# Optimization experiments

Measured on AMD Instinct MI355X. Metric: run time of the kernel, lower is better.

The kernel has to match this reference:

```python
import jax, jax.numpy as jnp
import numpy as np

D_MODEL = 1024
NUM_HEADS = 16
HEAD_DIM = D_MODEL // NUM_HEADS  # 64
ROPE_BASE = 10000.0


def setup_inputs() -> dict:
    key = jax.random.key(0)
    ks = jax.random.split(key, 12)
    B, S, D = 4, 2048, D_MODEL
    scale = 1.0 / np.sqrt(D)
    inp = {
        'query': jax.random.normal(ks[0], (B, S, D), jnp.float32),
        'key': jax.random.normal(ks[1], (B, S, D), jnp.float32),
        'value': jax.random.normal(ks[2], (B, S, D), jnp.float32),
        'Wq': jax.random.normal(ks[3], (D, D), jnp.float32) * scale,
        'bq': jnp.zeros((D,), jnp.float32),
        'Wk': jax.random.normal(ks[4], (D, D), jnp.float32) * scale,
        'bk': jnp.zeros((D,), jnp.float32),
        'Wv': jax.random.normal(ks[5], (D, D), jnp.float32) * scale,
        'bv': jnp.zeros((D,), jnp.float32),
        'Wo': jax.random.normal(ks[6], (D, D), jnp.float32) * scale,
        'bo': jnp.zeros((D,), jnp.float32),
    }
    return inp


def _rope_cos_sin(seq_len, head_dim, dtype):
    inv_freq = 1.0 / (ROPE_BASE ** (jnp.arange(0, head_dim, 2, dtype=jnp.float32) / head_dim))
    t = jnp.arange(seq_len, dtype=jnp.float32)
    freqs = jnp.einsum('i,j->ij', t, inv_freq)          # [S, hd/2]
    emb = jnp.concatenate([freqs, freqs], axis=-1)      # [S, hd]
    return jnp.cos(emb).astype(dtype), jnp.sin(emb).astype(dtype)


def _rotate_half(x):
    x1, x2 = jnp.split(x, 2, axis=-1)
    return jnp.concatenate([-x2, x1], axis=-1)


def reference(query, key, value, Wq, bq, Wk, bk, Wv, bv, Wo, bo):
    B, T, D = query.shape
    H, hd = NUM_HEADS, HEAD_DIM
    # projections -> [B, H, S, hd]
    Q = (query @ Wq + bq).reshape(B, T, H, hd).transpose(0, 2, 1, 3)
    K = (key @ Wk + bk).reshape(B, -1, H, hd).transpose(0, 2, 1, 3)
    V = (value @ Wv + bv).reshape(B, -1, H, hd).transpose(0, 2, 1, 3)
    # RoPE
    cos, sin = _rope_cos_sin(T, hd, Q.dtype)            # [S, hd]
    Q = Q * cos + _rotate_half(Q) * sin
    K = K * cos + _rotate_half(K) * sin
    # attention
    scores = jnp.einsum('bhtd,bhsd->bhts', Q, K) / jnp.sqrt(jnp.asarray(hd, Q.dtype))
    attn = jax.nn.softmax(scores, axis=-1)
    context = jnp.einsum('bhts,bhsd->bhtd', attn, V)
    context = context.transpose(0, 2, 1, 3).reshape(B, T, D)
    return context @ Wo + bo
```

## Files before the change

kernel.cpp:

```cpp
#include <hip/hip_runtime.h>
#include <hip/hip_bf16.h>
#include <cstdint>
#include <cstddef>

typedef __bf16 bf16_t;
typedef __bf16 bf16x8 __attribute__((ext_vector_type(8)));
typedef __bf16 bf16x4v __attribute__((ext_vector_type(4)));
typedef __bf16 bf16x2v __attribute__((ext_vector_type(2)));
typedef float f32x4 __attribute__((ext_vector_type(4)));
typedef float f32x16 __attribute__((ext_vector_type(16)));
typedef uint32_t u32x4 __attribute__((ext_vector_type(4)));
typedef uint32_t u32x2 __attribute__((ext_vector_type(2)));

#define DEVI static __device__ __forceinline__

DEVI void gl_lds16(const void* g, void* l) {
    __builtin_amdgcn_global_load_lds((const __attribute__((address_space(1))) void*)g,
                                     (__attribute__((address_space(3))) void*)l, 16, 0, 0);
}

DEVI float fexp2(float x) {
#if __has_builtin(__builtin_amdgcn_exp2f)
    return __builtin_amdgcn_exp2f(x);
#else
    return __expf(x * 0.6931471805599453f);
#endif
}

DEVI uint32_t pkbf16(float a, float b) {
    bf16x2v t;
    t[0] = (bf16_t)a;
    t[1] = (bf16_t)b;
    return __builtin_bit_cast(uint32_t, t);
}

__global__ __launch_bounds__(256) void castk(const float* __restrict__ i0, const float* __restrict__ i1,
                                             const float* __restrict__ i2, bf16_t* __restrict__ o0,
                                             bf16_t* __restrict__ o1, bf16_t* __restrict__ o2) {
    const float* in = blockIdx.y == 0 ? i0 : blockIdx.y == 1 ? i1 : i2;
    bf16_t* out = blockIdx.y == 0 ? o0 : blockIdx.y == 1 ? o1 : o2;
    size_t i = ((size_t)blockIdx.x * 256 + threadIdx.x) * 4;
    float4 v = *(const float4*)(in + i);
    bf16x4v o;
    o[0] = (bf16_t)v.x; o[1] = (bf16_t)v.y; o[2] = (bf16_t)v.z; o[3] = (bf16_t)v.w;
    *(bf16x4v*)(out + i) = o;
}

__global__ __launch_bounds__(256) void wtrans(const float* __restrict__ W0, const float* __restrict__ W1,
                                              const float* __restrict__ W2, const float* __restrict__ W3,
                                              bf16_t* __restrict__ O0, bf16_t* __restrict__ O1,
                                              bf16_t* __restrict__ O2, bf16_t* __restrict__ O3) {
    const float* W; bf16_t* O;
    switch (blockIdx.z) {
        case 0: W = W0; O = O0; break;
        case 1: W = W1; O = O1; break;
        case 2: W = W2; O = O2; break;
        default: W = W3; O = O3; break;
    }
    __shared__ float t[32][33];
    int tx = threadIdx.x & 31, ty = threadIdx.x >> 5;
    int bx = blockIdx.x * 32, by = blockIdx.y * 32;
#pragma unroll
    for (int yy = 0; yy < 4; ++yy)
        t[ty + yy * 8][tx] = W[(size_t)(by + ty + yy * 8) * 1024 + bx + tx];
    __syncthreads();
#pragma unroll
    for (int yy = 0; yy < 4; ++yy)
        O[(size_t)(bx + ty + yy * 8) * 1024 + by + tx] = (bf16_t)t[tx][ty + yy * 8];
}

__global__ __launch_bounds__(256) void rope_tab(float* __restrict__ ctab, float* __restrict__ stab) {
    int idx = blockIdx.x * 256 + threadIdx.x;
    int s = idx >> 5, i = idx & 31;
    float inv = 1.0f / powf(10000.0f, (float)i * (1.0f / 32.0f));
    float f = (float)s * inv;
    ctab[idx] = cosf(f);
    stab[idx] = sinf(f);
}

__global__ __launch_bounds__(256) void gemm_qkv(const bf16_t* __restrict__ Xq, const bf16_t* __restrict__ Xk,
                                                const bf16_t* __restrict__ Xv, const bf16_t* __restrict__ Wqt,
                                                const bf16_t* __restrict__ Wkt, const bf16_t* __restrict__ Wvt,
                                                const float* __restrict__ bqp, const float* __restrict__ bkp,
                                                const float* __restrict__ bvp, bf16_t* __restrict__ Qo,
                                                bf16_t* __restrict__ Ko, bf16_t* __restrict__ Vo,
                                                const float* __restrict__ ctab, const float* __restrict__ stab) {
    constexpr int K = 1024;
    const int z = blockIdx.z;
    const bf16_t* A  = z == 0 ? Xq : z == 1 ? Xk : Xv;
    const bf16_t* Bt = z == 0 ? Wqt : z == 1 ? Wkt : Wvt;
    const float* bias = z == 0 ? bqp : z == 1 ? bkp : bvp;
    bf16_t* O = z == 0 ? Qo : z == 1 ? Ko : Vo;
    const float scale = z == 0 ? 0.18033688011112042f : 1.0f;

    __shared__ alignas(16) bf16_t As[128 * 64];
    __shared__ alignas(16) bf16_t Bs[128 * 64];
    const int tid = threadIdx.x;
    const int w = tid >> 6, lane = tid & 63, c = lane & 15, qd = lane >> 4;
    const int wm = w >> 1, wn = w & 1;
    const int c7 = c & 7;
    const int m0 = blockIdx.x * 128, n0 = blockIdx.y * 128;
    f32x4 acc[4][4] = {};
    for (int kt = 0; kt < K / 64; ++kt) {
#pragma unroll
        for (int l = 0; l < 4; ++l) {
            int slot = l * 256 + tid;
            int row = slot >> 3, ch = slot & 7;
            int sch = ch ^ (row & 7);
            gl_lds16(A + (size_t)(m0 + row) * K + kt * 64 + sch * 8, (char*)As + (size_t)slot * 16);
            gl_lds16(Bt + (size_t)(n0 + row) * K + kt * 64 + sch * 8, (char*)Bs + (size_t)slot * 16);
        }
        __syncthreads();
#pragma unroll
        for (int kk = 0; kk < 2; ++kk) {
            const int cs8 = (kk * 4 + qd) ^ c7;
            bf16x8 af[4], bfr[4];
#pragma unroll
            for (int i = 0; i < 4; ++i)
                af[i] = *(const bf16x8*)&As[(wm * 64 + i * 16 + c) * 64 + cs8 * 8];
#pragma unroll
            for (int j = 0; j < 4; ++j)
                bfr[j] = *(const bf16x8*)&Bs[(wn * 64 + j * 16 + c) * 64 + cs8 * 8];
#pragma unroll
            for (int i = 0; i < 4; ++i)
#pragma unroll
                for (int j = 0; j < 4; ++j)
                    acc[i][j] = __builtin_amdgcn_mfma_f32_16x16x32_bf16(af[i], bfr[j], acc[i][j], 0, 0, 0);
        }
        __syncthreads();
    }
    const int mb = m0 + wm * 64;
    const int nb = n0 + wn * 64;
    const int h = nb >> 6;
    if (z == 2) {
#pragma unroll
        for (int i = 0; i < 4; ++i) {
            int m = mb + i * 16 + qd * 4;
            int b = m >> 11, s = m & 2047;
#pragma unroll
            for (int j = 0; j < 4; ++j) {
                int d = j * 16 + c;
                float bv = bias[nb + d];
                bf16x4v v4;
#pragma unroll
                for (int r = 0; r < 4; ++r) v4[r] = (bf16_t)(acc[i][j][r] + bv);
                *(bf16x4v*)(O + ((size_t)(b * 16 + h) * 64 + d) * 2048 + s) = v4;
            }
        }
    } else {
#pragma unroll
        for (int i = 0; i < 4; ++i)
#pragma unroll
            for (int jh = 0; jh < 2; ++jh) {
                int d1 = jh * 16 + c;
                float b1 = bias[nb + d1];
                float b2 = bias[nb + d1 + 32];
#pragma unroll
                for (int r = 0; r < 4; ++r) {
                    int m = mb + i * 16 + qd * 4 + r;
                    int b = m >> 11, s = m & 2047;
                    float v1 = acc[i][jh][r] + b1;
                    float v2 = acc[i][jh + 2][r] + b2;
                    float ct = ctab[s * 32 + d1];
                    float st = stab[s * 32 + d1];
                    size_t base = ((size_t)(b * 16 + h) * 2048 + s) * 64;
                    O[base + d1]      = (bf16_t)((v1 * ct - v2 * st) * scale);
                    O[base + d1 + 32] = (bf16_t)((v2 * ct + v1 * st) * scale);
                }
            }
    }
}

__global__ __launch_bounds__(256) void gemm_out(const bf16_t* __restrict__ A, const bf16_t* __restrict__ Bt,
                                                const float* __restrict__ bias, float* __restrict__ O) {
    constexpr int K = 1024, N = 1024;
    __shared__ alignas(16) bf16_t As[128 * 64];
    __shared__ alignas(16) bf16_t Bs[128 * 64];
    const int tid = threadIdx.x;
    const int w = tid >> 6, lane = tid & 63, c = lane & 15, qd = lane >> 4;
    const int wm = w >> 1, wn = w & 1;
    const int c7 = c & 7;
    const int m0 = blockIdx.x * 128, n0 = blockIdx.y * 128;
    f32x4 acc[4][4] = {};
    for (int kt = 0; kt < K / 64; ++kt) {
#pragma unroll
        for (int l = 0; l < 4; ++l) {
            int slot = l * 256 + tid;
            int row = slot >> 3, ch = slot & 7;
            int sch = ch ^ (row & 7);
            gl_lds16(A + (size_t)(m0 + row) * K + kt * 64 + sch * 8, (char*)As + (size_t)slot * 16);
            gl_lds16(Bt + (size_t)(n0 + row) * K + kt * 64 + sch * 8, (char*)Bs + (size_t)slot * 16);
        }
        __syncthreads();
#pragma unroll
        for (int kk = 0; kk < 2; ++kk) {
            const int cs8 = (kk * 4 + qd) ^ c7;
            bf16x8 af[4], bfr[4];
#pragma unroll
            for (int i = 0; i < 4; ++i)
                af[i] = *(const bf16x8*)&As[(wm * 64 + i * 16 + c) * 64 + cs8 * 8];
#pragma unroll
            for (int j = 0; j < 4; ++j)
                bfr[j] = *(const bf16x8*)&Bs[(wn * 64 + j * 16 + c) * 64 + cs8 * 8];
#pragma unroll
            for (int i = 0; i < 4; ++i)
#pragma unroll
                for (int j = 0; j < 4; ++j)
                    acc[i][j] = __builtin_amdgcn_mfma_f32_16x16x32_bf16(af[i], bfr[j], acc[i][j], 0, 0, 0);
        }
        __syncthreads();
    }
    const int mb = m0 + wm * 64, nb = n0 + wn * 64;
#pragma unroll
    for (int i = 0; i < 4; ++i)
#pragma unroll
        for (int j = 0; j < 4; ++j) {
            int n = nb + j * 16 + c;
            float bv = bias[n];
#pragma unroll
            for (int r = 0; r < 4; ++r) {
                int m = mb + i * 16 + qd * 4 + r;
                O[(size_t)m * N + n] = acc[i][j][r] + bv;
            }
        }
}

__global__ __launch_bounds__(256, 4) void attn(const bf16_t* __restrict__ Q, const bf16_t* __restrict__ K,
                                               const bf16_t* __restrict__ Vt, bf16_t* __restrict__ ctx) {
    constexpr int S = 2048, NT = S / 64;
    __shared__ alignas(16) char smem[32768];
    const int tid = threadIdx.x, w = tid >> 6, lane = tid & 63;
    const int lo5 = lane & 31, hi = lane >> 5;
    const int rm = (lo5 >> 1) & 7;
    const int bh = blockIdx.x, q0 = blockIdx.y * 128;
    const bf16_t* Qb = Q + (size_t)bh * S * 64 + (size_t)q0 * 64;
    const bf16_t* Kb = K + (size_t)bh * S * 64;
    const bf16_t* Vb = Vt + (size_t)bh * 64 * S;
#pragma unroll
    for (int l = 0; l < 4; ++l) {
        int slot = l * 256 + tid;
        int row = slot >> 3, ch = slot & 7;
        int sch = ch ^ ((row >> 1) & 7);
        gl_lds16(Qb + (size_t)row * 64 + sch * 8, smem + (size_t)slot * 16);
    }
    __syncthreads();
    bf16x8 qf[4];
    {
        const bf16_t* Qs = (const bf16_t*)smem;
#pragma unroll
        for (int kc = 0; kc < 4; ++kc)
            qf[kc] = *(const bf16x8*)&Qs[(size_t)(w * 32 + lo5) * 64 + ((kc * 2 + hi) ^ rm) * 8];
    }
    __syncthreads();
    auto stageK = [&](int kt, int buf) {
        const int s0 = kt * 64;
        char* kbase = smem + buf * 8192;
#pragma unroll
        for (int l = 0; l < 2; ++l) {
            int slot = l * 256 + tid;
            int row = slot >> 3, ch = slot & 7;
            int sch = ch ^ ((row >> 1) & 7);
            gl_lds16(Kb + (size_t)(s0 + row) * 64 + sch * 8, kbase + (size_t)slot * 16);
        }
    };
    auto stageV = [&](int kt, int buf) {
        const int s0 = kt * 64;
        char* vbase = smem + 16384 + buf * 8192;
#pragma unroll
        for (int l = 0; l < 2; ++l) {
            int slot = l * 256 + tid;
            int row = slot >> 3, ch = slot & 7;
            int sch = ch ^ ((row >> 1) & 7);
            gl_lds16(Vb + (size_t)row * S + s0 + sch * 8, vbase + (size_t)slot * 16);
        }
    };
    f32x16 acc_o[2] = {};
    f32x16 acc_l = {};
    const f32x16 Z16 = {};
    bf16x8 ones;
    {
        u32x4 ov = {0x3F803F80u, 0x3F803F80u, 0x3F803F80u, 0x3F803F80u};
        ones = __builtin_bit_cast(bf16x8, ov);
    }
    stageK(0, 0);
    __syncthreads();
    uint32_t pkuA[2][8] = {}, pkuB[2][8] = {};
    auto window = [&](int wi, uint32_t (&pkuP)[2][8], uint32_t (&pkuN)[2][8]) {
        if (wi + 1 < NT) stageK(wi + 1, (wi + 1) & 1);
        if (wi < NT) stageV(wi, wi & 1);
        f32x16 st[2];
        if (wi < NT) {
            const bf16_t* KsC = (const bf16_t*)(smem + (wi & 1) * 8192);
#pragma unroll
            for (int kc = 0; kc < 4; ++kc) {
                bf16x8 kf[2];
#pragma unroll
                for (int sb = 0; sb < 2; ++sb)
                    kf[sb] = *(const bf16x8*)&KsC[(size_t)(sb * 32 + lo5) * 64 + ((kc * 2 + hi) ^ rm) * 8];
#pragma unroll
                for (int sb = 0; sb < 2; ++sb)
                    st[sb] = __builtin_amdgcn_mfma_f32_32x32x16_bf16(kf[sb], qf[kc],
                                                                     kc == 0 ? Z16 : st[sb], 0, 0, 0);
            }
        }
        const bf16_t* VsC = (const bf16_t*)(smem + 16384 + ((wi - 1) & 1) * 8192);
#pragma unroll
        for (int skc = 0; skc < 4; ++skc) {
            const int sb = skc >> 1, b = (skc & 1) * 4;
            if (wi < NT) {
#pragma unroll
                for (int u = 0; u < 4; ++u)
                    pkuN[sb][b + u] = pkbf16(fexp2(st[sb][2 * (b + u)]), fexp2(st[sb][2 * (b + u) + 1]));
            }
            if (wi >= 1) {
                bf16x8 vf[2];
#pragma unroll
                for (int db = 0; db < 2; ++db)
                    vf[db] = *(const bf16x8*)&VsC[(size_t)(db * 32 + lo5) * 64 + ((skc * 2 + hi) ^ rm) * 8];
                uint32_t p0 = pkuP[sb][b + 0], p1 = pkuP[sb][b + 1];
                uint32_t p2 = pkuP[sb][b + 2], p3 = pkuP[sb][b + 3];
#if __has_builtin(__builtin_amdgcn_permlane32_swap)
                u32x2 r02 = __builtin_amdgcn_permlane32_swap(p0, p2, false, false);
                u32x2 r13 = __builtin_amdgcn_permlane32_swap(p1, p3, false, false);
                u32x4 av = {r02[0], r13[0], r02[1], r13[1]};
#else
                uint32_t send0 = hi ? p0 : p2;
                uint32_t send1 = hi ? p1 : p3;
                uint32_t recv0 = __shfl_xor(send0, 32);
                uint32_t recv1 = __shfl_xor(send1, 32);
                u32x4 av = {hi ? recv0 : p0, hi ? recv1 : p1,
                            hi ? p2 : recv0, hi ? p3 : recv1};
#endif
                bf16x8 af = __builtin_bit_cast(bf16x8, av);
                acc_l = __builtin_amdgcn_mfma_f32_32x32x16_bf16(af, ones, acc_l, 0, 0, 0);
#pragma unroll
                for (int db = 0; db < 2; ++db)
                    acc_o[db] = __builtin_amdgcn_mfma_f32_32x32x16_bf16(af, vf[db], acc_o[db], 0, 0, 0);
            }
        }
        __syncthreads();
    };
    for (int wi = 0; wi < NT; wi += 2) {
        window(wi, pkuB, pkuA);
        window(wi + 1, pkuA, pkuB);
    }
    window(NT, pkuB, pkuA);
    const int b = bh >> 4, h = bh & 15;
    float linv[16];
#pragma unroll
    for (int r = 0; r < 16; ++r) linv[r] = 1.0f / acc_l[r];
#pragma unroll
    for (int db = 0; db < 2; ++db)
#pragma unroll
        for (int r = 0; r < 16; ++r) {
            int qrow = q0 + w * 32 + (r & 3) + 8 * (r >> 2) + 4 * hi;
            int d = db * 32 + lo5;
            float o = acc_o[db][r] * linv[r];
            ctx[((size_t)(b * 2048 + qrow)) * 1024 + (size_t)h * 64 + d] = (bf16_t)o;
        }
}

extern "C" void kernel_launch(void* const* d_in, const int* in_sizes, int n_in,
                              void* d_out, int out_size, void* d_ws, size_t ws_size,
                              hipStream_t stream) {
    (void)in_sizes; (void)n_in; (void)out_size; (void)ws_size;
    const float* query = (const float*)d_in[0];
    const float* key   = (const float*)d_in[1];
    const float* value = (const float*)d_in[2];
    const float* Wq = (const float*)d_in[3];
    const float* bq = (const float*)d_in[4];
    const float* Wk = (const float*)d_in[5];
    const float* bk = (const float*)d_in[6];
    const float* Wv = (const float*)d_in[7];
    const float* bv = (const float*)d_in[8];
    const float* Wo = (const float*)d_in[9];
    const float* bo = (const float*)d_in[10];

    const size_t SZ = (size_t)8192 * 1024;
    bf16_t* Xq = (bf16_t*)d_ws;
    bf16_t* Xk = Xq + SZ;
    bf16_t* Xv = Xk + SZ;
    bf16_t* Qb = Xv + SZ;
    bf16_t* Kb = Qb + SZ;
    bf16_t* Vtb = Kb + SZ;
    bf16_t* Wqt = Vtb + SZ;
    bf16_t* Wkt = Wqt + 1024 * 1024;
    bf16_t* Wvt = Wkt + 1024 * 1024;
    bf16_t* Wot = Wvt + 1024 * 1024;
    float* ctab = (float*)(Wot + 1024 * 1024);
    float* stab = ctab + 2048 * 32;
    bf16_t* CT = Xq;

    castk<<<dim3(8192, 3), 256, 0, stream>>>(query, key, value, Xq, Xk, Xv);
    wtrans<<<dim3(32, 32, 4), 256, 0, stream>>>(Wq, Wk, Wv, Wo, Wqt, Wkt, Wvt, Wot);
    rope_tab<<<256, 256, 0, stream>>>(ctab, stab);
    gemm_qkv<<<dim3(64, 8, 3), 256, 0, stream>>>(Xq, Xk, Xv, Wqt, Wkt, Wvt, bq, bk, bv,
                                                 Qb, Kb, Vtb, ctab, stab);
    attn<<<dim3(64, 16), 256, 0, stream>>>(Qb, Kb, Vtb, CT);
    gemm_out<<<dim3(64, 8), 256, 0, stream>>>(CT, Wot, bo, (float*)d_out);
}
```

Baseline: 387.7 us.

## Interleave QK and PV MFMA halves, replace row-sum MFMA with scalar accumulation

Splits each attention window into two halves so the QK^T MFMAs for one 32-key block interleave with the PV MFMAs of the previous window. Window prologue and epilogue are specialised through a macro, which drops the runtime branches. The softmax denominator was computed with an extra MFMA against a ones vector; it is now accumulated as scalar sums of the exponentials and reduced with shuffles at the end. This removes one third of the PV-phase MFMAs and should improve overlap of exp/VALU work with matrix work, at the cost of more VALU adds and a dependence on permlane32_swap being available (the fallback path was removed).

```diff
diff --git a/kernel.cpp b/kernel.cpp
--- a/kernel.cpp
+++ b/kernel.cpp
@@ -275,80 +275,99 @@
         }
     };
     f32x16 acc_o[2] = {};
-    f32x16 acc_l = {};
+    float ls0 = 0.0f, ls1 = 0.0f;
     const f32x16 Z16 = {};
-    bf16x8 ones;
-    {
-        u32x4 ov = {0x3F803F80u, 0x3F803F80u, 0x3F803F80u, 0x3F803F80u};
-        ones = __builtin_bit_cast(bf16x8, ov);
-    }
+    uint32_t pkuA[2][8], pkuB[2][8];
     stageK(0, 0);
     __syncthreads();
-    uint32_t pkuA[2][8] = {}, pkuB[2][8] = {};
-    auto window = [&](int wi, uint32_t (&pkuP)[2][8], uint32_t (&pkuN)[2][8]) {
-        if (wi + 1 < NT) stageK(wi + 1, (wi + 1) & 1);
-        if (wi < NT) stageV(wi, wi & 1);
-        f32x16 st[2];
-        if (wi < NT) {
-            const bf16_t* KsC = (const bf16_t*)(smem + (wi & 1) * 8192);
-#pragma unroll
-            for (int kc = 0; kc < 4; ++kc) {
-                bf16x8 kf[2];
-#pragma unroll
-                for (int sb = 0; sb < 2; ++sb)
-                    kf[sb] = *(const bf16x8*)&KsC[(size_t)(sb * 32 + lo5) * 64 + ((kc * 2 + hi) ^ rm) * 8];
-#pragma unroll
-                for (int sb = 0; sb < 2; ++sb)
-                    st[sb] = __builtin_amdgcn_mfma_f32_32x32x16_bf16(kf[sb], qf[kc],
-                                                                     kc == 0 ? Z16 : st[sb], 0, 0, 0);
-            }
-        }
-        const bf16_t* VsC = (const bf16_t*)(smem + 16384 + ((wi - 1) & 1) * 8192);
-#pragma unroll
-        for (int skc = 0; skc < 4; ++skc) {
-            const int sb = skc >> 1, b = (skc & 1) * 4;
-            if (wi < NT) {
-#pragma unroll
-                for (int u = 0; u < 4; ++u)
-                    pkuN[sb][b + u] = pkbf16(fexp2(st[sb][2 * (b + u)]), fexp2(st[sb][2 * (b + u) + 1]));
-            }
-            if (wi >= 1) {
-                bf16x8 vf[2];
-#pragma unroll
-                for (int db = 0; db < 2; ++db)
-                    vf[db] = *(const bf16x8*)&VsC[(size_t)(db * 32 + lo5) * 64 + ((skc * 2 + hi) ^ rm) * 8];
-                uint32_t p0 = pkuP[sb][b + 0], p1 = pkuP[sb][b + 1];
-                uint32_t p2 = pkuP[sb][b + 2], p3 = pkuP[sb][b + 3];
-#if __has_builtin(__builtin_amdgcn_permlane32_swap)
-                u32x2 r02 = __builtin_amdgcn_permlane32_swap(p0, p2, false, false);
-                u32x2 r13 = __builtin_amdgcn_permlane32_swap(p1, p3, false, false);
-                u32x4 av = {r02[0], r13[0], r02[1], r13[1]};
-#else
-                uint32_t send0 = hi ? p0 : p2;
-                uint32_t send1 = hi ? p1 : p3;
-                uint32_t recv0 = __shfl_xor(send0, 32);
-                uint32_t recv1 = __shfl_xor(send1, 32);
-                u32x4 av = {hi ? recv0 : p0, hi ? recv1 : p1,
-                            hi ? p2 : recv0, hi ? p3 : recv1};
-#endif
-                bf16x8 af = __builtin_bit_cast(bf16x8, av);
-                acc_l = __builtin_amdgcn_mfma_f32_32x32x16_bf16(af, ones, acc_l, 0, 0, 0);
-#pragma unroll
-                for (int db = 0; db < 2; ++db)
-                    acc_o[db] = __builtin_amdgcn_mfma_f32_32x32x16_bf16(af, vf[db], acc_o[db], 0, 0, 0);
-            }
-        }
-        __syncthreads();
-    };
-    for (int wi = 0; wi < NT; wi += 2) {
-        window(wi, pkuB, pkuA);
-        window(wi + 1, pkuA, pkuB);
-    }
-    window(NT, pkuB, pkuA);
+
+#define ATTN_WIN(WI, PAR, DO_QK, DO_PV, STAGE_K, CONS, PROD)                              \
+    do {                                                                                   \
+        if (STAGE_K) stageK((WI) + 1, (PAR) ^ 1);                                          \
+        if (DO_QK) stageV((WI), (PAR));                                                    \
+        const bf16_t* KsC = (const bf16_t*)(smem + (PAR) * 8192);                          \
+        const bf16_t* VsC = (const bf16_t*)(smem + 16384 + ((PAR) ^ 1) * 8192);            \
+        f32x16 st0, st1;                                                                   \
+        if (DO_QK) {                                                                       \
+            _Pragma("unroll")                                                              \
+            for (int kc = 0; kc < 4; ++kc) {                                               \
+                bf16x8 kf = *(const bf16x8*)&KsC[(size_t)lo5 * 64 + ((kc * 2 + hi) ^ rm) * 8]; \
+                st0 = __builtin_amdgcn_mfma_f32_32x32x16_bf16(kf, qf[kc], kc == 0 ? Z16 : st0, 0, 0, 0); \
+            }                                                                              \
+            _Pragma("unroll")                                                              \
+            for (int u = 0; u < 8; ++u) {                                                  \
+                float e0 = fexp2(st0[2 * u]);                                              \
+                float e1 = fexp2(st0[2 * u + 1]);                                          \
+                PROD[0][u] = pkbf16(e0, e1);                                               \
+                if (u & 1) ls1 += e0 + e1; else ls0 += e0 + e1;                            \
+            }                                                                              \
+        }                                                                                  \
+        if (DO_PV) {                                                                       \
+            _Pragma("unroll")                                                              \
+            for (int skc = 0; skc < 2; ++skc) {                                            \
+                bf16x8 vf0 = *(const bf16x8*)&VsC[(size_t)lo5 * 64 + ((skc * 2 + hi) ^ rm) * 8];        \
+                bf16x8 vf1 = *(const bf16x8*)&VsC[(size_t)(32 + lo5) * 64 + ((skc * 2 + hi) ^ rm) * 8]; \
+                const int b = skc * 4;                                                     \
+                u32x2 r02 = __builtin_amdgcn_permlane32_swap(CONS[0][b + 0], CONS[0][b + 2], false, false); \
+                u32x2 r13 = __builtin_amdgcn_permlane32_swap(CONS[0][b + 1], CONS[0][b + 3], false, false); \
+                u32x4 av = {r02[0], r13[0], r02[1], r13[1]};                               \
+                bf16x8 af = __builtin_bit_cast(bf16x8, av);                                \
+                acc_o[0] = __builtin_amdgcn_mfma_f32_32x32x16_bf16(af, vf0, acc_o[0], 0, 0, 0); \
+                acc_o[1] = __builtin_amdgcn_mfma_f32_32x32x16_bf16(af, vf1, acc_o[1], 0, 0, 0); \
+            }                                                                              \
+        }                                                                                  \
+        if (DO_QK) {                                                                       \
+            _Pragma("unroll")                                                              \
+            for (int kc = 0; kc < 4; ++kc) {                                               \
+                bf16x8 kf = *(const bf16x8*)&KsC[(size_t)(32 + lo5) * 64 + ((kc * 2 + hi) ^ rm) * 8]; \
+                st1 = __builtin_amdgcn_mfma_f32_32x32x16_bf16(kf, qf[kc], kc == 0 ? Z16 : st1, 0, 0, 0); \
+            }                                                                              \
+            _Pragma("unroll")                                                              \
+            for (int u = 0; u < 8; ++u) {                                                  \
+                float e0 = fexp2(st1[2 * u]);                                              \
+                float e1 = fexp2(st1[2 * u + 1]);                                          \
+                PROD[1][u] = pkbf16(e0, e1);                                               \
+                if (u & 1) ls1 += e0 + e1; else ls0 += e0 + e1;                            \
+            }                                                                              \
+        }                                                                                  \
+        if (DO_PV) {                                                                       \
+            _Pragma("unroll")                                                              \
+            for (int skc = 2; skc < 4; ++skc) {                                            \
+                bf16x8 vf0 = *(const bf16x8*)&VsC[(size_t)lo5 * 64 + ((skc * 2 + hi) ^ rm) * 8];        \
+                bf16x8 vf1 = *(const bf16x8*)&VsC[(size_t)(32 + lo5) * 64 + ((skc * 2 + hi) ^ rm) * 8]; \
+                const int b = (skc & 1) * 4;                                               \
+                u32x2 r02 = __builtin_amdgcn_permlane32_swap(CONS[1][b + 0], CONS[1][b + 2], false, false); \
+                u32x2 r13 = __builtin_amdgcn_permlane32_swap(CONS[1][b + 1], CONS[1][b + 3], false, false); \
+                u32x4 av = {r02[0], r13[0], r02[1], r13[1]};                               \
+                bf16x8 af = __builtin_bit_cast(bf16x8, av);                                \
+                acc_o[0] = __builtin_amdgcn_mfma_f32_32x32x16_bf16(af, vf0, acc_o[0], 0, 0, 0); \
+                acc_o[1] = __builtin_amdgcn_mfma_f32_32x32x16_bf16(af, vf1, acc_o[1], 0, 0, 0); \
+            }                                                                              \
+        }                                                                                  \
+    } while (0)
+
+    ATTN_WIN(0, 0, true, false, true, pkuB, pkuA);
+    __syncthreads();
+    for (int wi = 1; wi < NT - 1; wi += 2) {
+        ATTN_WIN(wi, 1, true, true, true, pkuA, pkuB);
+        __syncthreads();
+        ATTN_WIN(wi + 1, 0, true, true, true, pkuB, pkuA);
+        __syncthreads();
+    }
+    ATTN_WIN(NT - 1, 1, true, true, false, pkuA, pkuB);
+    __syncthreads();
+    ATTN_WIN(NT, 0, false, true, false, pkuB, pkuA);
+#undef ATTN_WIN
+
+    float lsum = ls0 + ls1;
+    lsum += __shfl_xor(lsum, 32);
+    float linv[16];
+#pragma unroll
+    for (int r = 0; r < 16; ++r) {
+        int qr = (r & 3) + 8 * (r >> 2) + 4 * hi;
+        linv[r] = 1.0f / __shfl(lsum, qr);
+    }
     const int b = bh >> 4, h = bh & 15;
-    float linv[16];
-#pragma unroll
-    for (int r = 0; r < 16; ++r) linv[r] = 1.0f / acc_l[r];
 #pragma unroll
     for (int db = 0; db < 2; ++db)
 #pragma unroll
```

After: 363.9 us. -6.1%, faster.
